# Kernel optimization log

Measured on AMD Instinct MI355X. Metric: run time of the kernel, lower is better.

Reference implementation:

```python
import jax, jax.numpy as jnp
import numpy as np

B, L, E, D, A = 256, 196, 2048, 1024, 512


def setup_inputs() -> dict:
    key = jax.random.key(0)
    ks = jax.random.split(key, 9)
    enc_scale = 1.0 / np.sqrt(E)
    dec_scale = 1.0 / np.sqrt(D)
    att_scale = 1.0 / np.sqrt(A)
    return {
        "encoder_out": jax.random.normal(ks[0], (B, L, E), dtype=jnp.float32),
        "decoder_hidden": jax.random.normal(ks[1], (B, D), dtype=jnp.float32),
        "mask1": jax.random.randint(ks[2], (B, L), 0, 2, dtype=jnp.int32),
        "We": jax.random.uniform(ks[3], (E, A), jnp.float32, -enc_scale, enc_scale),
        "be": jax.random.uniform(ks[4], (A,), jnp.float32, -enc_scale, enc_scale),
        "Wd": jax.random.uniform(ks[5], (D, A), jnp.float32, -dec_scale, dec_scale),
        "bd": jax.random.uniform(ks[6], (A,), jnp.float32, -dec_scale, dec_scale),
        "wf": jax.random.uniform(ks[7], (A,), jnp.float32, -att_scale, att_scale),
        "bf": jax.random.uniform(ks[8], (), jnp.float32, -att_scale, att_scale),
    }


def reference(encoder_out, decoder_hidden, mask1, We, be, Wd, bd, wf, bf):
    # att1: [B, L, A]; att2: [B, A]
    att1 = jnp.einsum('ble,ea->bla', encoder_out, We) + be
    att2 = jnp.einsum('bd,da->ba', decoder_hidden, Wd) + bd
    # scores: [B, L]
    att = jnp.einsum('bla,a->bl', jnp.tanh(att1 + att2[:, None, :]), wf) + bf
    att = jnp.where(mask1 == 0, jnp.float32(-1e9), att)
    alpha = jax.nn.softmax(att, axis=1)
    # weighted sum over regions: [B, E]
    awe = jnp.einsum('ble,bl->be', encoder_out, alpha)
    return (awe, alpha)
```

## Files before the change

kernel.cpp:

```cpp
#include <hip/hip_runtime.h>
#include <hip/hip_bf16.h>


#define B_ 256
#define L_ 196
#define E_ 2048
#define D_ 1024
#define A_ 512
#define M_TOT (B_ * L_)

typedef __attribute__((ext_vector_type(8))) short bf16x8;
typedef __attribute__((ext_vector_type(4))) float f32x4;

static __device__ __forceinline__ unsigned short f2bf(float f) {
    union { float f; unsigned u; } u{f};
    unsigned r = u.u + 0x7fffu + ((u.u >> 16) & 1u);
    return (unsigned short)(r >> 16);
}

static __device__ __forceinline__ unsigned int pk2(float x, float y) {
    __hip_bfloat162 h = __float22bfloat162_rn(float2{x, y});
    return *reinterpret_cast<unsigned int*>(&h);
}

static __device__ __forceinline__ void gload_lds16(const void* g, void* l) {
    __builtin_amdgcn_global_load_lds(
        (const __attribute__((address_space(1))) unsigned int*)g,
        (__attribute__((address_space(3))) unsigned int*)l, 16, 0, 0);
}

__global__ __launch_bounds__(256) void k_wepack(const float* __restrict__ We,
                                                unsigned short* __restrict__ WeP) {
    int i = blockIdx.x * 256 + threadIdx.x;
    int k = i >> 9, n = i & 511;
    int kb = k >> 5, kg = (k >> 3) & 3, e = k & 7;
    int kgE = kg ^ ((n >> 1) & 3);
    WeP[(kb << 14) + (n << 5) + (kgE << 3) + e] = f2bf(We[i]);
}

__global__ __launch_bounds__(256) void k_bias2(const float* __restrict__ dec,
                                               const float* __restrict__ Wd,
                                               const float* __restrict__ be,
                                               const float* __restrict__ bd,
                                               float* __restrict__ bias2) {
    int b = blockIdx.x, t = threadIdx.x;
    __shared__ float ds[D_];
    for (int i = t; i < D_; i += 256) ds[i] = dec[b * D_ + i];
    __syncthreads();
    for (int a0 = 0; a0 < A_; a0 += 256) {
        int a = a0 + t;
        float acc = 0.f;
        #pragma unroll 8
        for (int d = 0; d < D_; d++) acc += ds[d] * Wd[d * A_ + a];
        bias2[b * A_ + a] = acc + be[a] + bd[a];
    }
}

__global__ __launch_bounds__(256, 3) void k_gemm_score(
        const float* __restrict__ enc,
        const unsigned short* __restrict__ WeP,
        const float* __restrict__ bias2,
        const float* __restrict__ wf,
        float* __restrict__ scoresP) {
    __shared__ __align__(16) unsigned short aL[2][128 * 32];
    __shared__ __align__(16) unsigned short bL[2][128 * 32];
    __shared__ float score_lds[4][64];

    const int tid = threadIdx.x;
    const int raw = blockIdx.x;
    const int wg = (raw & 7) * 196 + (raw >> 3);
    const int mt = wg >> 2, nt = wg & 3;
    const int m0 = mt * 128;

    const int lane = tid & 63;
    const int wid = tid >> 6;
    const int wm = wid >> 1, wn = wid & 1;
    const int kg = lane >> 4, lr = lane & 15;

    const int ar = tid >> 1, kh = tid & 1;
    const float* aSrc = enc + (size_t)(m0 + ar) * E_ + kh * 16;
    const int sw = (ar >> 1) & 3;
    const int aOff0 = ar * 32 + (((kh * 2 + 0) ^ sw) << 3);
    const int aOff1 = ar * 32 + (((kh * 2 + 1) ^ sw) << 3);

    const unsigned short* bSrcLane =
        WeP + nt * 4096 + (size_t)(wid * 1024 + lane * 8);

    auto stageB = [&](int kb, int buf) {
        const unsigned short* s = bSrcLane + ((size_t)kb << 14);
        #pragma unroll
        for (int c = 0; c < 2; c++)
            gload_lds16(s + c * 512, &bL[buf][(wid * 2 + c) * 512]);
    };
    auto loadA = [&](float4 (&v)[4], int t) {
        const float* p = aSrc + t * 32;
        v[0] = *reinterpret_cast<const float4*>(p);
        v[1] = *reinterpret_cast<const float4*>(p + 4);
        v[2] = *reinterpret_cast<const float4*>(p + 8);
        v[3] = *reinterpret_cast<const float4*>(p + 12);
    };
    auto writeA = [&](const float4 (&v)[4], int buf) {
        uint4 lo, hi;
        lo.x = pk2(v[0].x, v[0].y); lo.y = pk2(v[0].z, v[0].w);
        lo.z = pk2(v[1].x, v[1].y); lo.w = pk2(v[1].z, v[1].w);
        hi.x = pk2(v[2].x, v[2].y); hi.y = pk2(v[2].z, v[2].w);
        hi.z = pk2(v[3].x, v[3].y); hi.w = pk2(v[3].z, v[3].w);
        *reinterpret_cast<uint4*>(&aL[buf][aOff0]) = lo;
        *reinterpret_cast<uint4*>(&aL[buf][aOff1]) = hi;
    };

    f32x4 acc[4][4];
    #pragma unroll
    for (int i = 0; i < 4; i++)
        #pragma unroll
        for (int j = 0; j < 4; j++) acc[i][j] = (f32x4){0.f, 0.f, 0.f, 0.f};

    auto computeTile = [&](int buf) {
        bf16x8 bfr[4];
        #pragma unroll
        for (int j = 0; j < 4; j++) {
            int n = wn * 64 + j * 16 + lr;
            bfr[j] = *reinterpret_cast<const bf16x8*>(
                &bL[buf][n * 32 + ((kg ^ ((n >> 1) & 3)) << 3)]);
        }
        #pragma unroll
        for (int i = 0; i < 4; i++) {
            int row = wm * 64 + i * 16 + lr;
            bf16x8 af = *reinterpret_cast<const bf16x8*>(
                &aL[buf][row * 32 + ((kg ^ ((row >> 1) & 3)) << 3)]);
            #pragma unroll
            for (int j = 0; j < 4; j++)
                acc[i][j] = __builtin_amdgcn_mfma_f32_16x16x32_bf16(
                    af, bfr[j], acc[i][j], 0, 0, 0);
        }
    };

    stageB(0, 0);
    __builtin_amdgcn_sched_barrier(0);
    float4 av0[4], avH1[4], avH2[4];
    loadA(av0, 0);
    loadA(avH1, 1);
    loadA(avH2, 2);
    writeA(av0, 0);
    asm volatile("s_waitcnt vmcnt(8) lgkmcnt(0)" ::: "memory");
    __builtin_amdgcn_s_barrier();
    __builtin_amdgcn_sched_barrier(0);

    int buf = 0;
    for (int t = 0; t < 63; t++) {
        stageB(t + 1, buf ^ 1);
        __builtin_amdgcn_sched_barrier(0);
        int tn = (t + 3 > 63) ? 63 : t + 3;
        float4 avN[4];
        loadA(avN, tn);
        __builtin_amdgcn_sched_barrier(0);
        computeTile(buf);
        writeA(avH1, buf ^ 1);
        asm volatile("s_waitcnt vmcnt(4) lgkmcnt(0)" ::: "memory");
        __builtin_amdgcn_s_barrier();
        __builtin_amdgcn_sched_barrier(0);
        #pragma unroll
        for (int q = 0; q < 4; q++) { avH1[q] = avH2[q]; avH2[q] = avN[q]; }
        buf ^= 1;
    }
    computeTile(buf);

    #pragma unroll
    for (int i = 0; i < 4; i++) {
        #pragma unroll
        for (int r = 0; r < 4; r++) {
            int Rw = i * 16 + kg * 4 + r;
            int gm = m0 + wm * 64 + Rw;
            int bg = gm / L_;
            float sum = 0.f;
            #pragma unroll
            for (int j = 0; j < 4; j++) {
                int C = nt * 128 + wn * 64 + j * 16 + lr;
                float x = acc[i][j][r] + bias2[bg * A_ + C];
                float ex = __expf(2.f * x);
                sum += wf[C] * (1.f - 2.f * __builtin_amdgcn_rcpf(ex + 1.f));
            }
            #pragma unroll
            for (int mk = 1; mk < 16; mk <<= 1) sum += __shfl_xor(sum, mk);
            if (lr == 0) score_lds[wid][Rw] = sum;
        }
    }
    __syncthreads();
    if (tid < 128) {
        int wmp = tid >> 6;
        float s = score_lds[wmp * 2][tid & 63] + score_lds[wmp * 2 + 1][tid & 63];
        scoresP[nt * M_TOT + m0 + tid] = s;
    }
}

__global__ __launch_bounds__(256) void k_softmax(const float* __restrict__ scoresP,
                                                 const int* __restrict__ mask,
                                                 const float* __restrict__ bfp,
                                                 float* __restrict__ alpha) {
    int b = blockIdx.x, t = threadIdx.x;
    float bfv = bfp[0];
    float v = -INFINITY;
    if (t < L_) {
        int idx = b * L_ + t;
        float sc = scoresP[idx] + scoresP[M_TOT + idx] +
                   scoresP[2 * M_TOT + idx] + scoresP[3 * M_TOT + idx];
        v = (mask[idx] == 0) ? -1e9f : (sc + bfv);
    }
    __shared__ float redm[4], reds[4];
    float m = v;
    #pragma unroll
    for (int s = 1; s < 64; s <<= 1) m = fmaxf(m, __shfl_xor(m, s));
    int w = t >> 6;
    if ((t & 63) == 0) redm[w] = m;
    __syncthreads();
    m = fmaxf(fmaxf(redm[0], redm[1]), fmaxf(redm[2], redm[3]));
    float e = (t < L_) ? expf(v - m) : 0.f;
    float s = e;
    #pragma unroll
    for (int k = 1; k < 64; k <<= 1) s += __shfl_xor(s, k);
    if ((t & 63) == 0) reds[w] = s;
    __syncthreads();
    s = reds[0] + reds[1] + reds[2] + reds[3];
    if (t < L_) alpha[b * L_ + t] = e / s;
}

__global__ __launch_bounds__(512) void k_awe(const float* __restrict__ enc,
                                             const float* __restrict__ alpha,
                                             float* __restrict__ awe) {
    int b = blockIdx.x, t = threadIdx.x;
    __shared__ float al[L_];
    if (t < L_) al[t] = alpha[b * L_ + t];
    __syncthreads();
    const float* base = enc + (size_t)b * L_ * E_ + t * 4;
    float4 a0 = {0.f, 0.f, 0.f, 0.f}, a1 = a0, a2 = a0, a3 = a0;
    for (int l = 0; l < L_; l += 4) {
        float4 v0 = *reinterpret_cast<const float4*>(base + (size_t)l * E_);
        float4 v1 = *reinterpret_cast<const float4*>(base + (size_t)(l + 1) * E_);
        float4 v2 = *reinterpret_cast<const float4*>(base + (size_t)(l + 2) * E_);
        float4 v3 = *reinterpret_cast<const float4*>(base + (size_t)(l + 3) * E_);
        float c0 = al[l], c1 = al[l + 1], c2 = al[l + 2], c3 = al[l + 3];
        a0.x += c0 * v0.x; a0.y += c0 * v0.y; a0.z += c0 * v0.z; a0.w += c0 * v0.w;
        a1.x += c1 * v1.x; a1.y += c1 * v1.y; a1.z += c1 * v1.z; a1.w += c1 * v1.w;
        a2.x += c2 * v2.x; a2.y += c2 * v2.y; a2.z += c2 * v2.z; a2.w += c2 * v2.w;
        a3.x += c3 * v3.x; a3.y += c3 * v3.y; a3.z += c3 * v3.z; a3.w += c3 * v3.w;
    }
    float4 o;
    o.x = (a0.x + a1.x) + (a2.x + a3.x);
    o.y = (a0.y + a1.y) + (a2.y + a3.y);
    o.z = (a0.z + a1.z) + (a2.z + a3.z);
    o.w = (a0.w + a1.w) + (a2.w + a3.w);
    *reinterpret_cast<float4*>(awe + (size_t)b * E_ + t * 4) = o;
}

extern "C" void kernel_launch(void* const* d_in, const int* in_sizes, int n_in,
                              void* d_out, int out_size, void* d_ws, size_t ws_size,
                              hipStream_t stream) {
    const float* enc  = (const float*)d_in[0];
    const float* dec  = (const float*)d_in[1];
    const int*   mask = (const int*)d_in[2];
    const float* We   = (const float*)d_in[3];
    const float* be   = (const float*)d_in[4];
    const float* Wd   = (const float*)d_in[5];
    const float* bd   = (const float*)d_in[6];
    const float* wf   = (const float*)d_in[7];
    const float* bf   = (const float*)d_in[8];

    float* awe   = (float*)d_out;
    float* alpha = awe + (size_t)B_ * E_;

    char* ws = (char*)d_ws;
    unsigned short* WeP = (unsigned short*)ws;
    float* bias2   = (float*)(ws + (2u << 20));
    float* scoresP = (float*)(ws + (2u << 20) + (512u << 10));

    hipLaunchKernelGGL(k_wepack, dim3((E_ * A_) / 256), dim3(256), 0, stream, We, WeP);
    hipLaunchKernelGGL(k_bias2, dim3(B_), dim3(256), 0, stream, dec, Wd, be, bd, bias2);
    hipLaunchKernelGGL(k_gemm_score, dim3((M_TOT / 128) * 4), dim3(256), 0, stream,
                       enc, WeP, bias2, wf, scoresP);
    hipLaunchKernelGGL(k_softmax, dim3(B_), dim3(256), 0, stream, scoresP, mask, bf, alpha);
    hipLaunchKernelGGL(k_awe, dim3(B_), dim3(512), 0, stream, enc, alpha, awe);
}
```

Before: 450.1 us.

## Enlarge GEMM tiles to 256x256x64 and split awe reduction over L

The score GEMM moves from 128x128 tiles with K=32 steps to 256x256 tiles with K=64 steps, 512 threads and 8 waves. This halves the redundant reads of the fp32 encoder across N tiles (two N tiles instead of four) and raises MFMA work per barrier. The weight packing and LDS swizzle are reworked to match, and the A-prefetch depth drops from three stages to one. The awe kernel is split into four L-chunks per batch for more parallelism, with a new combine kernel that adds extra launch and workspace traffic.

```diff
diff --git a/kernel.cpp b/kernel.cpp
--- a/kernel.cpp
+++ b/kernel.cpp
@@ -33,9 +33,9 @@
                                                 unsigned short* __restrict__ WeP) {
     int i = blockIdx.x * 256 + threadIdx.x;
     int k = i >> 9, n = i & 511;
-    int kb = k >> 5, kg = (k >> 3) & 3, e = k & 7;
-    int kgE = kg ^ ((n >> 1) & 3);
-    WeP[(kb << 14) + (n << 5) + (kgE << 3) + e] = f2bf(We[i]);
+    int kb = k >> 6, slot = (k >> 3) & 7, e = k & 7;
+    int slotE = slot ^ (n & 7);
+    WeP[(kb << 15) + (n << 6) + (slotE << 3) + e] = f2bf(We[i]);
 }
 
 __global__ __launch_bounds__(256) void k_bias2(const float* __restrict__ dec,
@@ -56,126 +56,122 @@
     }
 }
 
-__global__ __launch_bounds__(256, 3) void k_gemm_score(
+__global__ __launch_bounds__(512, 2) void k_gemm_score(
         const float* __restrict__ enc,
         const unsigned short* __restrict__ WeP,
         const float* __restrict__ bias2,
         const float* __restrict__ wf,
         float* __restrict__ scoresP) {
-    __shared__ __align__(16) unsigned short aL[2][128 * 32];
-    __shared__ __align__(16) unsigned short bL[2][128 * 32];
-    __shared__ float score_lds[4][64];
+    __shared__ __align__(16) unsigned short aL[2][256 * 64];
+    __shared__ __align__(16) unsigned short bL[2][256 * 64];
+    __shared__ float score_lds[8][128];
 
     const int tid = threadIdx.x;
     const int raw = blockIdx.x;
-    const int wg = (raw & 7) * 196 + (raw >> 3);
-    const int mt = wg >> 2, nt = wg & 3;
-    const int m0 = mt * 128;
+    const int wg = (raw & 7) * 49 + (raw >> 3);
+    const int mt = wg >> 1, nt = wg & 1;
+    const int m0 = mt * 256;
 
     const int lane = tid & 63;
     const int wid = tid >> 6;
-    const int wm = wid >> 1, wn = wid & 1;
+    const int wm = wid >> 2, wn = wid & 3;
     const int kg = lane >> 4, lr = lane & 15;
 
     const int ar = tid >> 1, kh = tid & 1;
-    const float* aSrc = enc + (size_t)(m0 + ar) * E_ + kh * 16;
-    const int sw = (ar >> 1) & 3;
-    const int aOff0 = ar * 32 + (((kh * 2 + 0) ^ sw) << 3);
-    const int aOff1 = ar * 32 + (((kh * 2 + 1) ^ sw) << 3);
-
-    const unsigned short* bSrcLane =
-        WeP + nt * 4096 + (size_t)(wid * 1024 + lane * 8);
+    const float* aSrc = enc + (size_t)(m0 + ar) * E_ + kh * 32;
+
+    const unsigned short* bSrc = WeP + nt * 16384 + tid * 8;
 
     auto stageB = [&](int kb, int buf) {
-        const unsigned short* s = bSrcLane + ((size_t)kb << 14);
-        #pragma unroll
-        for (int c = 0; c < 2; c++)
-            gload_lds16(s + c * 512, &bL[buf][(wid * 2 + c) * 512]);
+        const unsigned short* s = bSrc + (kb << 15);
+        #pragma unroll
+        for (int c = 0; c < 4; c++)
+            gload_lds16(s + c * 4096, &bL[buf][c * 4096 + tid * 8]);
     };
-    auto loadA = [&](float4 (&v)[4], int t) {
-        const float* p = aSrc + t * 32;
-        v[0] = *reinterpret_cast<const float4*>(p);
-        v[1] = *reinterpret_cast<const float4*>(p + 4);
-        v[2] = *reinterpret_cast<const float4*>(p + 8);
-        v[3] = *reinterpret_cast<const float4*>(p + 12);
+    auto loadA = [&](float4 (&v)[8], int kb) {
+        const float* p = aSrc + (kb << 6);
+        #pragma unroll
+        for (int c = 0; c < 8; c++)
+            v[c] = *reinterpret_cast<const float4*>(p + c * 4);
     };
-    auto writeA = [&](const float4 (&v)[4], int buf) {
-        uint4 lo, hi;
-        lo.x = pk2(v[0].x, v[0].y); lo.y = pk2(v[0].z, v[0].w);
-        lo.z = pk2(v[1].x, v[1].y); lo.w = pk2(v[1].z, v[1].w);
-        hi.x = pk2(v[2].x, v[2].y); hi.y = pk2(v[2].z, v[2].w);
-        hi.z = pk2(v[3].x, v[3].y); hi.w = pk2(v[3].z, v[3].w);
-        *reinterpret_cast<uint4*>(&aL[buf][aOff0]) = lo;
-        *reinterpret_cast<uint4*>(&aL[buf][aOff1]) = hi;
-    };
-
-    f32x4 acc[4][4];
-    #pragma unroll
-    for (int i = 0; i < 4; i++)
-        #pragma unroll
-        for (int j = 0; j < 4; j++) acc[i][j] = (f32x4){0.f, 0.f, 0.f, 0.f};
-
-    auto computeTile = [&](int buf) {
-        bf16x8 bfr[4];
-        #pragma unroll
-        for (int j = 0; j < 4; j++) {
-            int n = wn * 64 + j * 16 + lr;
-            bfr[j] = *reinterpret_cast<const bf16x8*>(
-                &bL[buf][n * 32 + ((kg ^ ((n >> 1) & 3)) << 3)]);
-        }
-        #pragma unroll
-        for (int i = 0; i < 4; i++) {
-            int row = wm * 64 + i * 16 + lr;
-            bf16x8 af = *reinterpret_cast<const bf16x8*>(
-                &aL[buf][row * 32 + ((kg ^ ((row >> 1) & 3)) << 3)]);
-            #pragma unroll
-            for (int j = 0; j < 4; j++)
-                acc[i][j] = __builtin_amdgcn_mfma_f32_16x16x32_bf16(
-                    af, bfr[j], acc[i][j], 0, 0, 0);
+    auto writeA = [&](const float4 (&v)[8], int buf) {
+        #pragma unroll
+        for (int g = 0; g < 4; g++) {
+            uint4 q;
+            q.x = pk2(v[2 * g].x, v[2 * g].y);
+            q.y = pk2(v[2 * g].z, v[2 * g].w);
+            q.z = pk2(v[2 * g + 1].x, v[2 * g + 1].y);
+            q.w = pk2(v[2 * g + 1].z, v[2 * g + 1].w);
+            int slot = (kh * 4 + g) ^ (ar & 7);
+            *reinterpret_cast<uint4*>(&aL[buf][ar * 64 + slot * 8]) = q;
         }
     };
 
+    f32x4 acc[8][4];
+    #pragma unroll
+    for (int i = 0; i < 8; i++)
+        #pragma unroll
+        for (int j = 0; j < 4; j++) acc[i][j] = (f32x4){0.f, 0.f, 0.f, 0.f};
+
+    auto computeTile = [&](int buf) {
+        #pragma unroll
+        for (int ks = 0; ks < 2; ks++) {
+            bf16x8 bfr[4];
+            #pragma unroll
+            for (int j = 0; j < 4; j++) {
+                int n = wn * 64 + j * 16 + lr;
+                int slot = (ks * 4 + kg) ^ (n & 7);
+                bfr[j] = *reinterpret_cast<const bf16x8*>(
+                    &bL[buf][n * 64 + slot * 8]);
+            }
+            #pragma unroll
+            for (int i = 0; i < 8; i++) {
+                int row = wm * 128 + i * 16 + lr;
+                int slot = (ks * 4 + kg) ^ (row & 7);
+                bf16x8 af = *reinterpret_cast<const bf16x8*>(
+                    &aL[buf][row * 64 + slot * 8]);
+                #pragma unroll
+                for (int j = 0; j < 4; j++)
+                    acc[i][j] = __builtin_amdgcn_mfma_f32_16x16x32_bf16(
+                        af, bfr[j], acc[i][j], 0, 0, 0);
+            }
+        }
+    };
+
+    float4 av[8];
+    loadA(av, 0);
+    __builtin_amdgcn_sched_barrier(0);
     stageB(0, 0);
     __builtin_amdgcn_sched_barrier(0);
-    float4 av0[4], avH1[4], avH2[4];
-    loadA(av0, 0);
-    loadA(avH1, 1);
-    loadA(avH2, 2);
-    writeA(av0, 0);
-    asm volatile("s_waitcnt vmcnt(8) lgkmcnt(0)" ::: "memory");
-    __builtin_amdgcn_s_barrier();
-    __builtin_amdgcn_sched_barrier(0);
+    writeA(av, 0);
+    __syncthreads();
 
     int buf = 0;
-    for (int t = 0; t < 63; t++) {
-        stageB(t + 1, buf ^ 1);
+    for (int kb = 0; kb < 32; kb++) {
+        if (kb < 31) {
+            loadA(av, kb + 1);
+            __builtin_amdgcn_sched_barrier(0);
+            stageB(kb + 1, buf ^ 1);
+            __builtin_amdgcn_sched_barrier(0);
+        }
+        computeTile(buf);
         __builtin_amdgcn_sched_barrier(0);
-        int tn = (t + 3 > 63) ? 63 : t + 3;
-        float4 avN[4];
-        loadA(avN, tn);
-        __builtin_amdgcn_sched_barrier(0);
-        computeTile(buf);
-        writeA(avH1, buf ^ 1);
-        asm volatile("s_waitcnt vmcnt(4) lgkmcnt(0)" ::: "memory");
-        __builtin_amdgcn_s_barrier();
-        __builtin_amdgcn_sched_barrier(0);
-        #pragma unroll
-        for (int q = 0; q < 4; q++) { avH1[q] = avH2[q]; avH2[q] = avN[q]; }
+        if (kb < 31) writeA(av, buf ^ 1);
+        __syncthreads();
         buf ^= 1;
     }
-    computeTile(buf);
 
     #pragma unroll
-    for (int i = 0; i < 4; i++) {
+    for (int i = 0; i < 8; i++) {
         #pragma unroll
         for (int r = 0; r < 4; r++) {
             int Rw = i * 16 + kg * 4 + r;
-            int gm = m0 + wm * 64 + Rw;
+            int gm = m0 + wm * 128 + Rw;
             int bg = gm / L_;
             float sum = 0.f;
             #pragma unroll
             for (int j = 0; j < 4; j++) {
-                int C = nt * 128 + wn * 64 + j * 16 + lr;
+                int C = nt * 256 + wn * 64 + j * 16 + lr;
                 float x = acc[i][j][r] + bias2[bg * A_ + C];
                 float ex = __expf(2.f * x);
                 sum += wf[C] * (1.f - 2.f * __builtin_amdgcn_rcpf(ex + 1.f));
@@ -186,10 +182,11 @@
         }
     }
     __syncthreads();
-    if (tid < 128) {
-        int wmp = tid >> 6;
-        float s = score_lds[wmp * 2][tid & 63] + score_lds[wmp * 2 + 1][tid & 63];
-        scoresP[nt * M_TOT + m0 + tid] = s;
+    if (tid < 256) {
+        int wmp = tid >> 7, rl = tid & 127;
+        float s = score_lds[wmp * 4 + 0][rl] + score_lds[wmp * 4 + 1][rl] +
+                  score_lds[wmp * 4 + 2][rl] + score_lds[wmp * 4 + 3][rl];
+        scoresP[nt * M_TOT + m0 + wmp * 128 + rl] = s;
     }
 }
 
@@ -202,8 +199,7 @@
     float v = -INFINITY;
     if (t < L_) {
         int idx = b * L_ + t;
-        float sc = scoresP[idx] + scoresP[M_TOT + idx] +
-                   scoresP[2 * M_TOT + idx] + scoresP[3 * M_TOT + idx];
+        float sc = scoresP[idx] + scoresP[M_TOT + idx];
         v = (mask[idx] == 0) ? -1e9f : (sc + bfv);
     }
     __shared__ float redm[4], reds[4];
@@ -226,14 +222,16 @@
 
 __global__ __launch_bounds__(512) void k_awe(const float* __restrict__ enc,
                                              const float* __restrict__ alpha,
-                                             float* __restrict__ awe) {
-    int b = blockIdx.x, t = threadIdx.x;
-    __shared__ float al[L_];
-    if (t < L_) al[t] = alpha[b * L_ + t];
-    __syncthreads();
-    const float* base = enc + (size_t)b * L_ * E_ + t * 4;
+                                             float* __restrict__ aweP) {
+    int b = blockIdx.x >> 2, q = blockIdx.x & 3;
+    int t = threadIdx.x;
+    __shared__ float al[49];
+    if (t < 49) al[t] = alpha[b * L_ + q * 49 + t];
+    __syncthreads();
+    const float* base = enc + ((size_t)b * L_ + (size_t)q * 49) * E_ + t * 4;
     float4 a0 = {0.f, 0.f, 0.f, 0.f}, a1 = a0, a2 = a0, a3 = a0;
-    for (int l = 0; l < L_; l += 4) {
+    int l = 0;
+    for (; l + 4 <= 48; l += 4) {
         float4 v0 = *reinterpret_cast<const float4*>(base + (size_t)l * E_);
         float4 v1 = *reinterpret_cast<const float4*>(base + (size_t)(l + 1) * E_);
         float4 v2 = *reinterpret_cast<const float4*>(base + (size_t)(l + 2) * E_);
@@ -244,12 +242,31 @@
         a2.x += c2 * v2.x; a2.y += c2 * v2.y; a2.z += c2 * v2.z; a2.w += c2 * v2.w;
         a3.x += c3 * v3.x; a3.y += c3 * v3.y; a3.z += c3 * v3.z; a3.w += c3 * v3.w;
     }
+    {
+        float4 v0 = *reinterpret_cast<const float4*>(base + (size_t)48 * E_);
+        float c0 = al[48];
+        a0.x += c0 * v0.x; a0.y += c0 * v0.y; a0.z += c0 * v0.z; a0.w += c0 * v0.w;
+    }
     float4 o;
     o.x = (a0.x + a1.x) + (a2.x + a3.x);
     o.y = (a0.y + a1.y) + (a2.y + a3.y);
     o.z = (a0.z + a1.z) + (a2.z + a3.z);
     o.w = (a0.w + a1.w) + (a2.w + a3.w);
-    *reinterpret_cast<float4*>(awe + (size_t)b * E_ + t * 4) = o;
+    *reinterpret_cast<float4*>(aweP + ((size_t)q * B_ + b) * E_ + t * 4) = o;
+}
+
+__global__ __launch_bounds__(256) void k_awecomb(const float* __restrict__ aweP,
+                                                 float* __restrict__ awe) {
+    int i = blockIdx.x * 256 + threadIdx.x;
+    const float4* p = reinterpret_cast<const float4*>(aweP);
+    const size_t S = (size_t)B_ * E_ / 4;
+    float4 r0 = p[i], r1 = p[S + i], r2 = p[2 * S + i], r3 = p[3 * S + i];
+    float4 o;
+    o.x = (r0.x + r1.x) + (r2.x + r3.x);
+    o.y = (r0.y + r1.y) + (r2.y + r3.y);
+    o.z = (r0.z + r1.z) + (r2.z + r3.z);
+    o.w = (r0.w + r1.w) + (r2.w + r3.w);
+    reinterpret_cast<float4*>(awe)[i] = o;
 }
 
 extern "C" void kernel_launch(void* const* d_in, const int* in_sizes, int n_in,
@@ -272,11 +289,13 @@
     unsigned short* WeP = (unsigned short*)ws;
     float* bias2   = (float*)(ws + (2u << 20));
     float* scoresP = (float*)(ws + (2u << 20) + (512u << 10));
+    float* aweP    = (float*)(ws + (3u << 20));
 
     hipLaunchKernelGGL(k_wepack, dim3((E_ * A_) / 256), dim3(256), 0, stream, We, WeP);
     hipLaunchKernelGGL(k_bias2, dim3(B_), dim3(256), 0, stream, dec, Wd, be, bd, bias2);
-    hipLaunchKernelGGL(k_gemm_score, dim3((M_TOT / 128) * 4), dim3(256), 0, stream,
+    hipLaunchKernelGGL(k_gemm_score, dim3(392), dim3(512), 0, stream,
                        enc, WeP, bias2, wf, scoresP);
     hipLaunchKernelGGL(k_softmax, dim3(B_), dim3(256), 0, stream, scoresP, mask, bf, alpha);
-    hipLaunchKernelGGL(k_awe, dim3(B_), dim3(512), 0, stream, enc, alpha, awe);
-}
+    hipLaunchKernelGGL(k_awe, dim3(B_ * 4), dim3(512), 0, stream, enc, alpha, aweP);
+    hipLaunchKernelGGL(k_awecomb, dim3((B_ * E_ / 4) / 256), dim3(256), 0, stream, aweP, awe);
+}
```

Result: slower. 498.0 us (+10.6%).

## Triple-buffer GEMM LDS pipeline and split awe reduction across more blocks

Applied to the files above, without the earlier changes.

The GEMM-score kernel moves from double to triple-buffered LDS for the A and B tiles. B is staged two k-steps ahead and the loop is unrolled by three with rotating register sets, so more global loads stay in flight across each barrier. The awe kernel now splits the E dimension into 8 chunks per batch and the L dimension across 4 wavefronts, followed by an LDS reduction, which gives 2048 blocks instead of 256 for better parallelism. The cost is more LDS per GEMM block, which may lower occupancy, and an extra reduction step in awe.

```diff
diff --git a/kernel.cpp b/kernel.cpp
--- a/kernel.cpp
+++ b/kernel.cpp
@@ -17,12 +17,10 @@
     unsigned r = u.u + 0x7fffu + ((u.u >> 16) & 1u);
     return (unsigned short)(r >> 16);
 }
-
 static __device__ __forceinline__ unsigned int pk2(float x, float y) {
     __hip_bfloat162 h = __float22bfloat162_rn(float2{x, y});
     return *reinterpret_cast<unsigned int*>(&h);
 }
-
 static __device__ __forceinline__ void gload_lds16(const void* g, void* l) {
     __builtin_amdgcn_global_load_lds(
         (const __attribute__((address_space(1))) unsigned int*)g,
@@ -33,9 +31,9 @@
                                                 unsigned short* __restrict__ WeP) {
     int i = blockIdx.x * 256 + threadIdx.x;
     int k = i >> 9, n = i & 511;
-    int kb = k >> 5, kg = (k >> 3) & 3, e = k & 7;
-    int kgE = kg ^ ((n >> 1) & 3);
-    WeP[(kb << 14) + (n << 5) + (kgE << 3) + e] = f2bf(We[i]);
+    int kb = k >> 5, slot = (k >> 3) & 3, e = k & 7;
+    int slotE = slot ^ ((n >> 1) & 3);
+    WeP[(kb << 14) + (n << 5) + (slotE << 3) + e] = f2bf(We[i]);
 }
 
 __global__ __launch_bounds__(256) void k_bias2(const float* __restrict__ dec,
@@ -62,8 +60,8 @@
         const float* __restrict__ bias2,
         const float* __restrict__ wf,
         float* __restrict__ scoresP) {
-    __shared__ __align__(16) unsigned short aL[2][128 * 32];
-    __shared__ __align__(16) unsigned short bL[2][128 * 32];
+    __shared__ __align__(16) unsigned short aL[3][4096];
+    __shared__ __align__(16) unsigned short bL[3][4096];
     __shared__ float score_lds[4][64];
 
     const int tid = threadIdx.x;
@@ -72,41 +70,38 @@
     const int mt = wg >> 2, nt = wg & 3;
     const int m0 = mt * 128;
 
-    const int lane = tid & 63;
-    const int wid = tid >> 6;
+    const int lane = tid & 63, wid = tid >> 6;
     const int wm = wid >> 1, wn = wid & 1;
     const int kg = lane >> 4, lr = lane & 15;
 
     const int ar = tid >> 1, kh = tid & 1;
     const float* aSrc = enc + (size_t)(m0 + ar) * E_ + kh * 16;
     const int sw = (ar >> 1) & 3;
-    const int aOff0 = ar * 32 + (((kh * 2 + 0) ^ sw) << 3);
-    const int aOff1 = ar * 32 + (((kh * 2 + 1) ^ sw) << 3);
-
-    const unsigned short* bSrcLane =
-        WeP + nt * 4096 + (size_t)(wid * 1024 + lane * 8);
+    const int aOff0 = ar * 32 + ((((kh << 1) | 0) ^ sw) << 3);
+    const int aOff1 = ar * 32 + ((((kh << 1) | 1) ^ sw) << 3);
+
+    const unsigned short* bSrc = WeP + nt * 4096 + tid * 8;
 
     auto stageB = [&](int kb, int buf) {
-        const unsigned short* s = bSrcLane + ((size_t)kb << 14);
-        #pragma unroll
-        for (int c = 0; c < 2; c++)
-            gload_lds16(s + c * 512, &bL[buf][(wid * 2 + c) * 512]);
-    };
-    auto loadA = [&](float4 (&v)[4], int t) {
-        const float* p = aSrc + t * 32;
+        const unsigned short* s = bSrc + (kb << 14);
+        gload_lds16(s,        &bL[buf][tid * 8]);
+        gload_lds16(s + 2048, &bL[buf][2048 + tid * 8]);
+    };
+    auto loadA = [&](float4 (&v)[4], int kb) {
+        const float* p = aSrc + (kb << 5);
         v[0] = *reinterpret_cast<const float4*>(p);
         v[1] = *reinterpret_cast<const float4*>(p + 4);
         v[2] = *reinterpret_cast<const float4*>(p + 8);
         v[3] = *reinterpret_cast<const float4*>(p + 12);
     };
     auto writeA = [&](const float4 (&v)[4], int buf) {
-        uint4 lo, hi;
-        lo.x = pk2(v[0].x, v[0].y); lo.y = pk2(v[0].z, v[0].w);
-        lo.z = pk2(v[1].x, v[1].y); lo.w = pk2(v[1].z, v[1].w);
-        hi.x = pk2(v[2].x, v[2].y); hi.y = pk2(v[2].z, v[2].w);
-        hi.z = pk2(v[3].x, v[3].y); hi.w = pk2(v[3].z, v[3].w);
-        *reinterpret_cast<uint4*>(&aL[buf][aOff0]) = lo;
-        *reinterpret_cast<uint4*>(&aL[buf][aOff1]) = hi;
+        uint4 q0, q1;
+        q0.x = pk2(v[0].x, v[0].y); q0.y = pk2(v[0].z, v[0].w);
+        q0.z = pk2(v[1].x, v[1].y); q0.w = pk2(v[1].z, v[1].w);
+        q1.x = pk2(v[2].x, v[2].y); q1.y = pk2(v[2].z, v[2].w);
+        q1.z = pk2(v[3].x, v[3].y); q1.w = pk2(v[3].z, v[3].w);
+        *reinterpret_cast<uint4*>(&aL[buf][aOff0]) = q0;
+        *reinterpret_cast<uint4*>(&aL[buf][aOff1]) = q1;
     };
 
     f32x4 acc[4][4];
@@ -135,35 +130,54 @@
         }
     };
 
+    float4 avA[4], avB[4], avC[4];
+    int t = 0;
+
+    auto step = [&](float4 (&wr)[4], float4 (&ld)[4],
+                    int sbuf, int cbuf, int wbuf) {
+        stageB(t + 2, sbuf);
+        __builtin_amdgcn_sched_barrier(0);
+        loadA(ld, t + 3);
+        __builtin_amdgcn_sched_barrier(0);
+        computeTile(cbuf);
+        writeA(wr, wbuf);
+        asm volatile("s_waitcnt vmcnt(6) lgkmcnt(0)" ::: "memory");
+        __builtin_amdgcn_s_barrier();
+        __builtin_amdgcn_sched_barrier(0);
+        t++;
+    };
+
     stageB(0, 0);
-    __builtin_amdgcn_sched_barrier(0);
-    float4 av0[4], avH1[4], avH2[4];
-    loadA(av0, 0);
-    loadA(avH1, 1);
-    loadA(avH2, 2);
-    writeA(av0, 0);
+    stageB(1, 1);
+    __builtin_amdgcn_sched_barrier(0);
+    loadA(avA, 0);
+    loadA(avB, 1);
+    loadA(avC, 2);
+    __builtin_amdgcn_sched_barrier(0);
+    writeA(avA, 0);
     asm volatile("s_waitcnt vmcnt(8) lgkmcnt(0)" ::: "memory");
     __builtin_amdgcn_s_barrier();
     __builtin_amdgcn_sched_barrier(0);
 
-    int buf = 0;
-    for (int t = 0; t < 63; t++) {
-        stageB(t + 1, buf ^ 1);
-        __builtin_amdgcn_sched_barrier(0);
-        int tn = (t + 3 > 63) ? 63 : t + 3;
-        float4 avN[4];
-        loadA(avN, tn);
-        __builtin_amdgcn_sched_barrier(0);
-        computeTile(buf);
-        writeA(avH1, buf ^ 1);
-        asm volatile("s_waitcnt vmcnt(4) lgkmcnt(0)" ::: "memory");
-        __builtin_amdgcn_s_barrier();
-        __builtin_amdgcn_sched_barrier(0);
-        #pragma unroll
-        for (int q = 0; q < 4; q++) { avH1[q] = avH2[q]; avH2[q] = avN[q]; }
-        buf ^= 1;
-    }
-    computeTile(buf);
+    for (int u = 0; u < 20; u++) {
+        step(avB, avA, 2, 0, 1);
+        step(avC, avB, 0, 1, 2);
+        step(avA, avC, 1, 2, 0);
+    }
+    step(avB, avA, 2, 0, 1);
+    stageB(63, 0);
+    __builtin_amdgcn_sched_barrier(0);
+    computeTile(1);
+    writeA(avC, 2);
+    asm volatile("s_waitcnt vmcnt(6) lgkmcnt(0)" ::: "memory");
+    __builtin_amdgcn_s_barrier();
+    __builtin_amdgcn_sched_barrier(0);
+    computeTile(2);
+    writeA(avA, 0);
+    asm volatile("s_waitcnt vmcnt(0) lgkmcnt(0)" ::: "memory");
+    __builtin_amdgcn_s_barrier();
+    __builtin_amdgcn_sched_barrier(0);
+    computeTile(0);
 
     #pragma unroll
     for (int i = 0; i < 4; i++) {
@@ -187,9 +201,9 @@
     }
     __syncthreads();
     if (tid < 128) {
-        int wmp = tid >> 6;
-        float s = score_lds[wmp * 2][tid & 63] + score_lds[wmp * 2 + 1][tid & 63];
-        scoresP[nt * M_TOT + m0 + tid] = s;
+        int wmp = tid >> 6, rl = tid & 63;
+        float s = score_lds[wmp * 2][rl] + score_lds[wmp * 2 + 1][rl];
+        scoresP[nt * M_TOT + m0 + wmp * 64 + rl] = s;
     }
 }
 
@@ -224,32 +238,36 @@
     if (t < L_) alpha[b * L_ + t] = e / s;
 }
 
-__global__ __launch_bounds__(512) void k_awe(const float* __restrict__ enc,
+__global__ __launch_bounds__(256) void k_awe(const float* __restrict__ enc,
                                              const float* __restrict__ alpha,
                                              float* __restrict__ awe) {
-    int b = blockIdx.x, t = threadIdx.x;
+    int b = blockIdx.y, ec = blockIdx.x, t = threadIdx.x;
+    int g = t >> 6, lt = t & 63;
     __shared__ float al[L_];
+    __shared__ float4 red[256];
     if (t < L_) al[t] = alpha[b * L_ + t];
     __syncthreads();
-    const float* base = enc + (size_t)b * L_ * E_ + t * 4;
-    float4 a0 = {0.f, 0.f, 0.f, 0.f}, a1 = a0, a2 = a0, a3 = a0;
-    for (int l = 0; l < L_; l += 4) {
-        float4 v0 = *reinterpret_cast<const float4*>(base + (size_t)l * E_);
-        float4 v1 = *reinterpret_cast<const float4*>(base + (size_t)(l + 1) * E_);
-        float4 v2 = *reinterpret_cast<const float4*>(base + (size_t)(l + 2) * E_);
-        float4 v3 = *reinterpret_cast<const float4*>(base + (size_t)(l + 3) * E_);
-        float c0 = al[l], c1 = al[l + 1], c2 = al[l + 2], c3 = al[l + 3];
-        a0.x += c0 * v0.x; a0.y += c0 * v0.y; a0.z += c0 * v0.z; a0.w += c0 * v0.w;
-        a1.x += c1 * v1.x; a1.y += c1 * v1.y; a1.z += c1 * v1.z; a1.w += c1 * v1.w;
-        a2.x += c2 * v2.x; a2.y += c2 * v2.y; a2.z += c2 * v2.z; a2.w += c2 * v2.w;
-        a3.x += c3 * v3.x; a3.y += c3 * v3.y; a3.z += c3 * v3.z; a3.w += c3 * v3.w;
-    }
-    float4 o;
-    o.x = (a0.x + a1.x) + (a2.x + a3.x);
-    o.y = (a0.y + a1.y) + (a2.y + a3.y);
-    o.z = (a0.z + a1.z) + (a2.z + a3.z);
-    o.w = (a0.w + a1.w) + (a2.w + a3.w);
-    *reinterpret_cast<float4*>(awe + (size_t)b * E_ + t * 4) = o;
+    int e0 = (ec << 8) + (lt << 2);
+    const float* base = enc + (size_t)b * L_ * E_ + e0;
+    float4 acc = {0.f, 0.f, 0.f, 0.f};
+    int l0 = g * 49;
+    #pragma unroll 7
+    for (int l = l0; l < l0 + 49; l++) {
+        float4 v = *reinterpret_cast<const float4*>(base + (size_t)l * E_);
+        float a = al[l];
+        acc.x += a * v.x; acc.y += a * v.y; acc.z += a * v.z; acc.w += a * v.w;
+    }
+    red[t] = acc;
+    __syncthreads();
+    if (t < 64) {
+        float4 r0 = red[t], r1 = red[64 + t], r2 = red[128 + t], r3 = red[192 + t];
+        float4 o;
+        o.x = r0.x + r1.x + r2.x + r3.x;
+        o.y = r0.y + r1.y + r2.y + r3.y;
+        o.z = r0.z + r1.z + r2.z + r3.z;
+        o.w = r0.w + r1.w + r2.w + r3.w;
+        *reinterpret_cast<float4*>(awe + b * E_ + (ec << 8) + (t << 2)) = o;
+    }
 }
 
 extern "C" void kernel_launch(void* const* d_in, const int* in_sizes, int n_in,
@@ -270,13 +288,13 @@
 
     char* ws = (char*)d_ws;
     unsigned short* WeP = (unsigned short*)ws;
-    float* bias2   = (float*)(ws + (2u << 20));
-    float* scoresP = (float*)(ws + (2u << 20) + (512u << 10));
+    float* bias2   = (float*)(ws + 2097152);
+    float* scoresP = (float*)(ws + 2621440);
 
     hipLaunchKernelGGL(k_wepack, dim3((E_ * A_) / 256), dim3(256), 0, stream, We, WeP);
     hipLaunchKernelGGL(k_bias2, dim3(B_), dim3(256), 0, stream, dec, Wd, be, bd, bias2);
-    hipLaunchKernelGGL(k_gemm_score, dim3((M_TOT / 128) * 4), dim3(256), 0, stream,
+    hipLaunchKernelGGL(k_gemm_score, dim3(1568), dim3(256), 0, stream,
                        enc, WeP, bias2, wf, scoresP);
     hipLaunchKernelGGL(k_softmax, dim3(B_), dim3(256), 0, stream, scoresP, mask, bf, alpha);
-    hipLaunchKernelGGL(k_awe, dim3(B_), dim3(512), 0, stream, enc, alpha, awe);
-}
+    hipLaunchKernelGGL(k_awe, dim3(8, B_), dim3(256), 0, stream, enc, alpha, awe);
+}
```

Result: faster. 437.6 us (-2.8%).
